# Kernel tuning notes

Measured on AMD Instinct MI355X. Metric: run time of the kernel, lower is better.

Reference implementation:

```python
import jax, jax.numpy as jnp
import numpy as np

N = 100000      # nodes
E = 1250000     # edges
IN = 128        # in_channels
H = 64          # hidden_channels
L = 2           # num_layers (GCNConv count)
EPS = 1e-5      # BatchNorm eps


def setup_inputs() -> dict:
    key = jax.random.key(0)
    ks = jax.random.split(key, 10)
    x = jax.random.normal(ks[0], (N, IN), jnp.float32)
    edge_index = jax.random.randint(ks[1], (2, E), 0, N, dtype=jnp.int32)
    fc_w = jax.random.normal(ks[2], (IN, H), jnp.float32) / np.sqrt(IN)
    fc_b = jax.random.normal(ks[3], (H,), jnp.float32) * 0.01
    conv_w = jax.random.normal(ks[4], (L, H, H), jnp.float32) / np.sqrt(H)
    conv_b = jax.random.normal(ks[5], (L, H), jnp.float32) * 0.01
    bn_gamma = jnp.ones((L + 1, H), jnp.float32)
    bn_beta = jnp.zeros((L + 1, H), jnp.float32)
    bn_mean = jax.random.normal(ks[6], (L + 1, H), jnp.float32) * 0.1
    bn_var = jax.random.uniform(ks[7], (L + 1, H), jnp.float32) + 0.5
    return {"x": x, "edge_index": edge_index, "fc_w": fc_w, "fc_b": fc_b,
            "conv_w": conv_w, "conv_b": conv_b, "bn_gamma": bn_gamma,
            "bn_beta": bn_beta, "bn_mean": bn_mean, "bn_var": bn_var}


def reference(x, edge_index, fc_w, fc_b, conv_w, conv_b, bn_gamma, bn_beta, bn_mean, bn_var):
    n = x.shape[0]
    loops = jnp.arange(n, dtype=edge_index.dtype)
    src = jnp.concatenate([edge_index[0], loops])   # add self-loops (GCNConv default)
    dst = jnp.concatenate([edge_index[1], loops])
    # symmetric normalization: deg computed on destination, norm = d_s^-1/2 * d_d^-1/2
    deg = jax.ops.segment_sum(jnp.ones_like(dst, x.dtype), dst, num_segments=n)
    dis = jax.lax.rsqrt(deg)                        # deg >= 1 thanks to self-loops
    norm = dis[src] * dis[dst]                      # [E+N]

    def bn(h, i):  # eval-mode BatchNorm1d with running stats
        return (h - bn_mean[i]) * (bn_gamma[i] * jax.lax.rsqrt(bn_var[i] + EPS)) + bn_beta[i]

    h = jax.nn.relu(bn(x @ fc_w + fc_b, 0))         # [N, H]; dropout is identity in eval
    last = h
    for i in range(conv_w.shape[0]):
        hw = h @ conv_w[i]                          # GCNConv: transform then aggregate
        agg = jax.ops.segment_sum(hw[src] * norm[:, None], dst, num_segments=n) + conv_b[i]
        h = jax.nn.relu(bn(agg, i + 1)) + last      # residual to post-fc activation
    return h
```

## Files before the change

### kernel.cpp

```cpp
#include <hip/hip_runtime.h>

#define NNODES 100000
#define NEDGES 1250000
#define IN_CH 128
#define HID 64
#define BN_EPS 1e-5f

#define NPAD 100352
#define DRANGE 12500
#define FILL_CHUNK 4096
#define FILL_CHUNKS 306
#define GBLOCKS 3125
#define ELL_C 32
#define OVF_CAP 65536

typedef __attribute__((ext_vector_type(8))) short s16x8;
typedef __attribute__((ext_vector_type(4))) float f32x4;

__device__ __forceinline__ ushort f2bf(float f) {
    union { float f; unsigned int i; } c;
    c.f = f;
    unsigned int lsb = (c.i >> 16) & 1u;
    return (ushort)((c.i + 0x7FFFu + lsb) >> 16);
}
__device__ __forceinline__ float bf2f(ushort u) {
    union { unsigned int i; float f; } c;
    c.i = (unsigned int)u << 16;
    return c.f;
}
__device__ __forceinline__ float asf(unsigned int i) {
    union { unsigned int i; float f; } c;
    c.i = i;
    return c.f;
}

__global__ void csr_fill(const int* __restrict__ src, const int* __restrict__ dst,
                         int* cnt, int* __restrict__ ell,
                         int* ovf_n, int2* __restrict__ ovf) {
    int p = blockIdx.x & 7;
    int base = (blockIdx.x >> 3) * (FILL_CHUNK / 4);
    int lo = p * DRANGE, hi = lo + DRANGE;
    const int4* dst4 = (const int4*)dst;
    const int4* src4 = (const int4*)src;
#pragma unroll
    for (int k = 0; k < FILL_CHUNK / 1024; ++k) {
        int i = base + k * 256 + threadIdx.x;
        if (i < NEDGES / 4) {
            int4 dv = dst4[i];
            int4 sv = src4[i];
#define FILL_ONE(D, S)                                                      \
            if ((D) >= lo && (D) < hi) {                                    \
                int slot = atomicAdd(&cnt[(D)], 1);                         \
                if (slot < ELL_C) ell[((D) << 5) + slot] = (S) << 7;        \
                else {                                                      \
                    int oi = atomicAdd(ovf_n, 1);                           \
                    if (oi < OVF_CAP) ovf[oi] = make_int2((D), (S) << 7);   \
                }                                                           \
            }
            FILL_ONE(dv.x, sv.x)
            FILL_ONE(dv.y, sv.y)
            FILL_ONE(dv.z, sv.z)
            FILL_ONE(dv.w, sv.w)
#undef FILL_ONE
        }
    }
}

__global__ __launch_bounds__(256) void fc_bn_relu(
        const float* __restrict__ x, const float* __restrict__ w,
        const float* __restrict__ b,
        const float* __restrict__ g, const float* __restrict__ be,
        const float* __restrict__ mu, const float* __restrict__ var,
        const int* __restrict__ cnt, float* __restrict__ dis,
        ushort* __restrict__ h0) {
    const int wave = threadIdx.x >> 6;
    const int lane = threadIdx.x & 63;
    const int m = lane & 15;
    const int q = lane >> 4;
    const int node_base = (blockIdx.x * 4 + wave) * 16;

    if (m == 0) {
#pragma unroll
        for (int r = 0; r < 4; ++r) {
            int node = node_base + q * 4 + r;
            if (node < NNODES) dis[node] = rsqrtf((float)(cnt[node] + 1));
        }
    }

    s16x8 bfrag[4][4];
#pragma unroll
    for (int kc = 0; kc < 4; ++kc)
#pragma unroll
        for (int ct = 0; ct < 4; ++ct)
#pragma unroll
            for (int j = 0; j < 8; ++j)
                bfrag[kc][ct][j] = (short)f2bf(w[(kc * 32 + q * 8 + j) * HID + ct * 16 + m]);

    f32x4 acc[4] = {{0,0,0,0},{0,0,0,0},{0,0,0,0},{0,0,0,0}};

    int row = node_base + m;
    if (row >= NNODES) row = NNODES - 1;
    const float4* xp = (const float4*)(x + (size_t)row * IN_CH + q * 8);

#pragma unroll
    for (int kc = 0; kc < 4; ++kc) {
        float4 a0 = xp[kc * 8 + 0];
        float4 a1 = xp[kc * 8 + 1];
        s16x8 af;
        af[0] = (short)f2bf(a0.x); af[1] = (short)f2bf(a0.y);
        af[2] = (short)f2bf(a0.z); af[3] = (short)f2bf(a0.w);
        af[4] = (short)f2bf(a1.x); af[5] = (short)f2bf(a1.y);
        af[6] = (short)f2bf(a1.z); af[7] = (short)f2bf(a1.w);
#pragma unroll
        for (int ct = 0; ct < 4; ++ct)
            acc[ct] = __builtin_amdgcn_mfma_f32_16x16x32_bf16(af, bfrag[kc][ct], acc[ct], 0, 0, 0);
    }

#pragma unroll
    for (int ct = 0; ct < 4; ++ct) {
        int col = ct * 16 + m;
        float sc = g[col] * rsqrtf(var[col] + BN_EPS);
        float off = (b[col] - mu[col]) * sc + be[col];
#pragma unroll
        for (int r = 0; r < 4; ++r) {
            int node = node_base + q * 4 + r;
            if (node < NNODES)
                h0[(size_t)node * HID + col] =
                    f2bf(fmaxf(acc[ct][r] * sc + off, 0.f));
        }
    }
}

__global__ __launch_bounds__(256) void conv_mm(
        const ushort* __restrict__ h, const float* __restrict__ w,
        const float* __restrict__ dis, ushort* __restrict__ hws) {
    const int wave = threadIdx.x >> 6;
    const int lane = threadIdx.x & 63;
    const int m = lane & 15;
    const int q = lane >> 4;
    const int node_base = (blockIdx.x * 4 + wave) * 16;

    s16x8 bfrag[2][4];
#pragma unroll
    for (int kc = 0; kc < 2; ++kc)
#pragma unroll
        for (int ct = 0; ct < 4; ++ct)
#pragma unroll
            for (int j = 0; j < 8; ++j)
                bfrag[kc][ct][j] = (short)f2bf(w[(kc * 32 + q * 8 + j) * HID + ct * 16 + m]);

    f32x4 acc[4] = {{0,0,0,0},{0,0,0,0},{0,0,0,0},{0,0,0,0}};

    int row = node_base + m;
    if (row >= NNODES) row = NNODES - 1;

#pragma unroll
    for (int kc = 0; kc < 2; ++kc) {
        const s16x8* hp = (const s16x8*)(h + (size_t)row * HID + kc * 32 + q * 8);
        s16x8 af = *hp;
#pragma unroll
        for (int ct = 0; ct < 4; ++ct)
            acc[ct] = __builtin_amdgcn_mfma_f32_16x16x32_bf16(af, bfrag[kc][ct], acc[ct], 0, 0, 0);
    }

    float dv[4];
#pragma unroll
    for (int r = 0; r < 4; ++r) {
        int node = node_base + q * 4 + r;
        dv[r] = (node < NNODES) ? dis[node] : 0.f;
    }
#pragma unroll
    for (int ct = 0; ct < 4; ++ct) {
#pragma unroll
        for (int r = 0; r < 4; ++r) {
            int node = node_base + q * 4 + r;
            if (node < NNODES)
                hws[(size_t)node * HID + ct * 16 + m] = f2bf(acc[ct][r] * dv[r]);
        }
    }
}

__global__ __launch_bounds__(256) void gather_update(
        const ushort* __restrict__ hws,
        const int* __restrict__ cnt, const int* __restrict__ ell,
        const int* __restrict__ ovf_n, const int2* __restrict__ ovf,
        const float* __restrict__ dis,
        const float* __restrict__ bias,
        const float* __restrict__ g, const float* __restrict__ be,
        const float* __restrict__ mu, const float* __restrict__ var,
        const ushort* __restrict__ last,
        ushort* __restrict__ out_bf, float* __restrict__ out_f,
        int write_f32) {
    const int wave = threadIdx.x >> 6;
    const int lane = threadIdx.x & 63;
    const int grp  = lane >> 3;
    const int j    = lane & 7;
    const int d = blockIdx.x * 32 + wave * 8 + grp;
    const unsigned int moff = (unsigned int)j * 16u;
    const unsigned int doff = ((unsigned int)d << 7) + moff;

    const char* hb = (const char*)hws;

    float a[8];
    {
        uint4 sv = *(const uint4*)(hb + doff);
        a[0] = asf(sv.x << 16); a[1] = asf(sv.x & 0xffff0000u);
        a[2] = asf(sv.y << 16); a[3] = asf(sv.y & 0xffff0000u);
        a[4] = asf(sv.z << 16); a[5] = asf(sv.z & 0xffff0000u);
        a[6] = asf(sv.w << 16); a[7] = asf(sv.w & 0xffff0000u);
    }

#define ACC8(V)                                                         \
    a[0] += asf((V).x << 16); a[1] += asf((V).x & 0xffff0000u);         \
    a[2] += asf((V).y << 16); a[3] += asf((V).y & 0xffff0000u);         \
    a[4] += asf((V).z << 16); a[5] += asf((V).z & 0xffff0000u);         \
    a[6] += asf((V).w << 16); a[7] += asf((V).w & 0xffff0000u);

    const int n = cnt[d];
    const int nn = (n < ELL_C) ? n : ELL_C;
    const int* sp = ell + ((size_t)d << 5);

    int k = 0;
    for (; k + 8 <= nn; k += 8) {
        unsigned int o0 = (unsigned int)sp[k + 0] + moff;
        unsigned int o1 = (unsigned int)sp[k + 1] + moff;
        unsigned int o2 = (unsigned int)sp[k + 2] + moff;
        unsigned int o3 = (unsigned int)sp[k + 3] + moff;
        unsigned int o4 = (unsigned int)sp[k + 4] + moff;
        unsigned int o5 = (unsigned int)sp[k + 5] + moff;
        unsigned int o6 = (unsigned int)sp[k + 6] + moff;
        unsigned int o7 = (unsigned int)sp[k + 7] + moff;
        uint4 v0 = *(const uint4*)(hb + o0);
        uint4 v1 = *(const uint4*)(hb + o1);
        uint4 v2 = *(const uint4*)(hb + o2);
        uint4 v3 = *(const uint4*)(hb + o3);
        uint4 v4 = *(const uint4*)(hb + o4);
        uint4 v5 = *(const uint4*)(hb + o5);
        uint4 v6 = *(const uint4*)(hb + o6);
        uint4 v7 = *(const uint4*)(hb + o7);
        ACC8(v0) ACC8(v1) ACC8(v2) ACC8(v3)
        ACC8(v4) ACC8(v5) ACC8(v6) ACC8(v7)
    }
    for (; k + 4 <= nn; k += 4) {
        unsigned int o0 = (unsigned int)sp[k + 0] + moff;
        unsigned int o1 = (unsigned int)sp[k + 1] + moff;
        unsigned int o2 = (unsigned int)sp[k + 2] + moff;
        unsigned int o3 = (unsigned int)sp[k + 3] + moff;
        uint4 v0 = *(const uint4*)(hb + o0);
        uint4 v1 = *(const uint4*)(hb + o1);
        uint4 v2 = *(const uint4*)(hb + o2);
        uint4 v3 = *(const uint4*)(hb + o3);
        ACC8(v0) ACC8(v1) ACC8(v2) ACC8(v3)
    }
    for (; k < nn; ++k) {
        uint4 v = *(const uint4*)(hb + ((unsigned int)sp[k] + moff));
        ACC8(v)
    }
    if (n > ELL_C) {
        int on = *ovf_n;
        if (on > OVF_CAP) on = OVF_CAP;
        for (int jj = 0; jj < on; ++jj) {
            int2 e = ovf[jj];
            if (e.x == d) {
                uint4 v = *(const uint4*)(hb + ((unsigned int)e.y + moff));
                ACC8(v)
            }
        }
    }
#undef ACC8

    float dd = dis[d];
    float4 bi0 = ((const float4*)bias)[2 * j], bi1 = ((const float4*)bias)[2 * j + 1];
    float4 g0  = ((const float4*)g)[2 * j],    g1  = ((const float4*)g)[2 * j + 1];
    float4 be0 = ((const float4*)be)[2 * j],   be1 = ((const float4*)be)[2 * j + 1];
    float4 mu0 = ((const float4*)mu)[2 * j],   mu1 = ((const float4*)mu)[2 * j + 1];
    float4 va0 = ((const float4*)var)[2 * j],  va1 = ((const float4*)var)[2 * j + 1];
    uint4 lv = *(const uint4*)((const char*)last + doff);
    float l0 = asf(lv.x << 16), l1 = asf(lv.x & 0xffff0000u);
    float l2 = asf(lv.y << 16), l3 = asf(lv.y & 0xffff0000u);
    float l4 = asf(lv.z << 16), l5 = asf(lv.z & 0xffff0000u);
    float l6 = asf(lv.w << 16), l7 = asf(lv.w & 0xffff0000u);

#define EPI(A, BI, GV, BE, MU, VA, LO) \
    (fmaxf(((A) * dd + (BI) - (MU)) * ((GV) * rsqrtf((VA) + BN_EPS)) + (BE), 0.f) + (LO))
    float r0 = EPI(a[0], bi0.x, g0.x, be0.x, mu0.x, va0.x, l0);
    float r1 = EPI(a[1], bi0.y, g0.y, be0.y, mu0.y, va0.y, l1);
    float r2 = EPI(a[2], bi0.z, g0.z, be0.z, mu0.z, va0.z, l2);
    float r3 = EPI(a[3], bi0.w, g0.w, be0.w, mu0.w, va0.w, l3);
    float r4 = EPI(a[4], bi1.x, g1.x, be1.x, mu1.x, va1.x, l4);
    float r5 = EPI(a[5], bi1.y, g1.y, be1.y, mu1.y, va1.y, l5);
    float r6 = EPI(a[6], bi1.z, g1.z, be1.z, mu1.z, va1.z, l6);
    float r7 = EPI(a[7], bi1.w, g1.w, be1.w, mu1.w, va1.w, l7);
#undef EPI

    if (write_f32) {
        float4* op = (float4*)(out_f + (size_t)d * HID + j * 8);
        op[0] = make_float4(r0, r1, r2, r3);
        op[1] = make_float4(r4, r5, r6, r7);
    } else {
        uint4 o;
        o.x = (unsigned int)f2bf(r0) | ((unsigned int)f2bf(r1) << 16);
        o.y = (unsigned int)f2bf(r2) | ((unsigned int)f2bf(r3) << 16);
        o.z = (unsigned int)f2bf(r4) | ((unsigned int)f2bf(r5) << 16);
        o.w = (unsigned int)f2bf(r6) | ((unsigned int)f2bf(r7) << 16);
        *(uint4*)((char*)out_bf + doff) = o;
    }
}

extern "C" void kernel_launch(void* const* d_in, const int* in_sizes, int n_in,
                              void* d_out, int out_size, void* d_ws, size_t ws_size,
                              hipStream_t stream) {
    const float* x      = (const float*)d_in[0];
    const int*   eidx   = (const int*)d_in[1];
    const float* fc_w   = (const float*)d_in[2];
    const float* fc_b   = (const float*)d_in[3];
    const float* conv_w = (const float*)d_in[4];
    const float* conv_b = (const float*)d_in[5];
    const float* bn_g   = (const float*)d_in[6];
    const float* bn_b   = (const float*)d_in[7];
    const float* bn_m   = (const float*)d_in[8];
    const float* bn_v   = (const float*)d_in[9];

    const int* src = eidx;
    const int* dst = eidx + NEDGES;

    float* out = (float*)d_out;

    float*  dis     = (float*)d_ws;
    int*    cnt     = (int*)(dis + NPAD);
    int*    ovf_n   = cnt + NPAD;
    int2*   ovf     = (int2*)(ovf_n + 4);
    int*    ell     = (int*)(ovf + OVF_CAP);
    ushort* h0      = (ushort*)(ell + (size_t)NNODES * ELL_C);
    ushort* h1      = h0 + (size_t)NNODES * HID;
    ushort* hws     = h1 + (size_t)NNODES * HID;

    const int BLK = 256;
    const int gridF   = FILL_CHUNKS * 8;
    const int gridMM  = (NNODES + 63) / 64;

    hipMemsetAsync(cnt, 0, (size_t)NPAD * 4 + 16, stream);

    csr_fill<<<gridF, BLK, 0, stream>>>(src, dst, cnt, ell, ovf_n, ovf);

    fc_bn_relu<<<gridMM, BLK, 0, stream>>>(x, fc_w, fc_b, bn_g, bn_b, bn_m, bn_v,
                                           cnt, dis, h0);

    conv_mm<<<gridMM, BLK, 0, stream>>>(h0, conv_w, dis, hws);
    gather_update<<<GBLOCKS, BLK, 0, stream>>>(hws, cnt, ell, ovf_n, ovf, dis,
                                               conv_b, bn_g + HID, bn_b + HID,
                                               bn_m + HID, bn_v + HID, h0,
                                               h1, nullptr, 0);

    conv_mm<<<gridMM, BLK, 0, stream>>>(h1, conv_w + HID * HID, dis, hws);
    gather_update<<<GBLOCKS, BLK, 0, stream>>>(hws, cnt, ell, ovf_n, ovf, dis,
                                               conv_b + HID, bn_g + 2 * HID, bn_b + 2 * HID,
                                               bn_m + 2 * HID, bn_v + 2 * HID, h0,
                                               nullptr, out, 1);
}
```

Measured before the change: 307.6 us.

## Replace 8-pass edge scan with LDS binning by destination range then ELL fill

The old fill kernel read the full edge list eight times, once per destination range, to keep atomics localized. The new version reads edges once, bins them per destination range in shared memory, and writes packed (local dst, src) words to staging buffers reusing the hws workspace. A second kernel then fills the ELL table range by range. This cuts repeated edge reads at the cost of an extra staging write/read, an extra launch, and LDS atomics.

```diff
diff --git a/kernel.cpp b/kernel.cpp
--- a/kernel.cpp
+++ b/kernel.cpp
@@ -8,8 +8,11 @@
 
 #define NPAD 100352
 #define DRANGE 12500
-#define FILL_CHUNK 4096
-#define FILL_CHUNKS 306
+#define BIN_CHUNK 2048
+#define BIN_BLOCKS 611
+#define BIN_CAP_LDS 384
+#define BIN_REGION 312500
+#define FILL_BLOCKS 512
 #define GBLOCKS 3125
 #define ELL_C 32
 #define OVF_CAP 65536
@@ -34,34 +37,96 @@
     return c.f;
 }
 
-__global__ void csr_fill(const int* __restrict__ src, const int* __restrict__ dst,
-                         int* cnt, int* __restrict__ ell,
-                         int* ovf_n, int2* __restrict__ ovf) {
-    int p = blockIdx.x & 7;
-    int base = (blockIdx.x >> 3) * (FILL_CHUNK / 4);
-    int lo = p * DRANGE, hi = lo + DRANGE;
+__device__ __forceinline__ void fill_direct(int d, int soff, int* cnt,
+                                            int* ell, int* ovf_n, int2* ovf) {
+    int slot = atomicAdd(&cnt[d], 1);
+    if (slot < ELL_C) ell[(d << 5) + slot] = soff;
+    else {
+        int oi = atomicAdd(ovf_n, 1);
+        if (oi < OVF_CAP) ovf[oi] = make_int2(d, soff);
+    }
+}
+
+__global__ __launch_bounds__(256) void edge_bin(
+        const int* __restrict__ src, const int* __restrict__ dst,
+        unsigned int* __restrict__ staged, int* bin_n,
+        int* cnt, int* __restrict__ ell, int* ovf_n, int2* __restrict__ ovf) {
+    __shared__ unsigned int sbin[8][BIN_CAP_LDS];
+    __shared__ int scnt[8];
+    __shared__ int sbase[8];
+    const int tid = threadIdx.x;
+    if (tid < 8) scnt[tid] = 0;
+    __syncthreads();
+
+    const int base = blockIdx.x * (BIN_CHUNK / 4);
     const int4* dst4 = (const int4*)dst;
     const int4* src4 = (const int4*)src;
 #pragma unroll
-    for (int k = 0; k < FILL_CHUNK / 1024; ++k) {
-        int i = base + k * 256 + threadIdx.x;
+    for (int k = 0; k < BIN_CHUNK / 1024; ++k) {
+        int i = base + k * 256 + tid;
         if (i < NEDGES / 4) {
             int4 dv = dst4[i];
             int4 sv = src4[i];
-#define FILL_ONE(D, S)                                                      \
-            if ((D) >= lo && (D) < hi) {                                    \
-                int slot = atomicAdd(&cnt[(D)], 1);                         \
-                if (slot < ELL_C) ell[((D) << 5) + slot] = (S) << 7;        \
-                else {                                                      \
-                    int oi = atomicAdd(ovf_n, 1);                           \
-                    if (oi < OVF_CAP) ovf[oi] = make_int2((D), (S) << 7);   \
-                }                                                           \
+#define BIN_ONE(D, S)                                                       \
+            {                                                               \
+                int b_ = (D) / DRANGE;                                      \
+                unsigned int pk_ = ((unsigned int)((D) - b_ * DRANGE) << 17)\
+                                   | (unsigned int)(S);                     \
+                int sl_ = atomicAdd(&scnt[b_], 1);                          \
+                if (sl_ < BIN_CAP_LDS) sbin[b_][sl_] = pk_;                 \
+                else fill_direct((D), (S) << 7, cnt, ell, ovf_n, ovf);      \
             }
-            FILL_ONE(dv.x, sv.x)
-            FILL_ONE(dv.y, sv.y)
-            FILL_ONE(dv.z, sv.z)
-            FILL_ONE(dv.w, sv.w)
-#undef FILL_ONE
+            BIN_ONE(dv.x, sv.x)
+            BIN_ONE(dv.y, sv.y)
+            BIN_ONE(dv.z, sv.z)
+            BIN_ONE(dv.w, sv.w)
+#undef BIN_ONE
+        }
+    }
+    __syncthreads();
+    if (tid < 8) {
+        int c = scnt[tid];
+        if (c > BIN_CAP_LDS) c = BIN_CAP_LDS;
+        sbase[tid] = atomicAdd(&bin_n[tid], c);
+    }
+    __syncthreads();
+#pragma unroll
+    for (int b = 0; b < 8; ++b) {
+        int c = scnt[b];
+        if (c > BIN_CAP_LDS) c = BIN_CAP_LDS;
+        int gb = sbase[b];
+        for (int i = tid; i < c; i += 256) {
+            int g = gb + i;
+            unsigned int v = sbin[b][i];
+            if (g < BIN_REGION) {
+                staged[(size_t)b * BIN_REGION + g] = v;
+            } else {
+                int d = b * DRANGE + (int)(v >> 17);
+                fill_direct(d, (int)(v & 0x1FFFFu) << 7, cnt, ell, ovf_n, ovf);
+            }
+        }
+    }
+}
+
+__global__ __launch_bounds__(256) void ell_fill(
+        const unsigned int* __restrict__ staged, const int* __restrict__ bin_n,
+        int* cnt, int* __restrict__ ell, int* ovf_n, int2* __restrict__ ovf) {
+    const int p  = blockIdx.x & 7;
+    const int bi = blockIdx.x >> 3;
+    const int nb = FILL_BLOCKS / 8;
+    int n = bin_n[p];
+    if (n > BIN_REGION) n = BIN_REGION;
+    const unsigned int* sp = staged + (size_t)p * BIN_REGION;
+    const int lo = p * DRANGE;
+    for (int i = bi * 256 + threadIdx.x; i < n; i += nb * 256) {
+        unsigned int v = sp[i];
+        int d = lo + (int)(v >> 17);
+        int soff = (int)(v & 0x1FFFFu) << 7;
+        int slot = atomicAdd(&cnt[d], 1);
+        if (slot < ELL_C) ell[(d << 5) + slot] = soff;
+        else {
+            int oi = atomicAdd(ovf_n, 1);
+            if (oi < OVF_CAP) ovf[oi] = make_int2(d, soff);
         }
     }
 }
@@ -328,20 +393,25 @@
 
     float*  dis     = (float*)d_ws;
     int*    cnt     = (int*)(dis + NPAD);
-    int*    ovf_n   = cnt + NPAD;
-    int2*   ovf     = (int2*)(ovf_n + 4);
+    int*    meta    = cnt + NPAD;
+    int*    ovf_n   = meta;
+    int*    bin_n   = meta + 8;
+    int2*   ovf     = (int2*)(meta + 16);
     int*    ell     = (int*)(ovf + OVF_CAP);
     ushort* h0      = (ushort*)(ell + (size_t)NNODES * ELL_C);
     ushort* h1      = h0 + (size_t)NNODES * HID;
     ushort* hws     = h1 + (size_t)NNODES * HID;
+    unsigned int* staged = (unsigned int*)hws;
 
     const int BLK = 256;
-    const int gridF   = FILL_CHUNKS * 8;
     const int gridMM  = (NNODES + 63) / 64;
 
-    hipMemsetAsync(cnt, 0, (size_t)NPAD * 4 + 16, stream);
-
-    csr_fill<<<gridF, BLK, 0, stream>>>(src, dst, cnt, ell, ovf_n, ovf);
+    hipMemsetAsync(cnt, 0, (size_t)NPAD * 4 + 64, stream);
+
+    edge_bin<<<BIN_BLOCKS, BLK, 0, stream>>>(src, dst, staged, bin_n,
+                                             cnt, ell, ovf_n, ovf);
+    ell_fill<<<FILL_BLOCKS, BLK, 0, stream>>>(staged, bin_n,
+                                              cnt, ell, ovf_n, ovf);
 
     fc_bn_relu<<<gridMM, BLK, 0, stream>>>(x, fc_w, fc_b, bn_g, bn_b, bn_m, bn_v,
                                            cnt, dis, h0);
```

Result: no change. 312.4 us (+1.6%).
